# Kernel tuning notes

Measured on AMD Instinct MI355X. Metric: run time of the kernel, lower is better.

## Reference

```python
import jax, jax.numpy as jnp
import numpy as np

B = 4096
HASH_BITS = 128
TEACHER_DIM = 768
TEMPERATURE = 0.2
CONTRASTIVE_W = 1.0
DISTILL_W = 0.5
QUANT_W = 0.01


def _l2_normalize(x, eps=1e-12):
    # matches torch F.normalize(dim=-1)
    n = jnp.sqrt(jnp.sum(x * x, axis=-1, keepdims=True))
    return x / jnp.maximum(n, eps)


def setup_inputs() -> dict:
    key = jax.random.key(0)
    k1, k2, k3, k4 = jax.random.split(key, 4)
    logits = jax.random.normal(k1, (B, HASH_BITS), dtype=jnp.float32)
    # binary {-1,+1} codes as in the module contract
    hash_codes = jnp.sign(jax.random.normal(k2, (B, HASH_BITS), dtype=jnp.float32))
    hash_codes = jnp.where(hash_codes == 0, 1.0, hash_codes)
    teacher_embed = jax.random.normal(k3, (B, TEACHER_DIM), dtype=jnp.float32)
    # sparse random positives plus self-positives (guarantees each row nonempty)
    rand_pos = jax.random.uniform(k4, (B, B)) < 0.002
    eye = jnp.eye(B, dtype=bool)
    positive_mask = rand_pos | eye
    return {
        "logits": logits,
        "hash_codes": hash_codes,
        "teacher_embed": teacher_embed,
        "positive_mask": positive_mask,
    }


def reference(logits, hash_codes, teacher_embed, positive_mask):
    teacher = _l2_normalize(teacher_embed)

    # ---- contrastive (vectorized form of the per-row python loop) ----
    ln = _l2_normalize(logits)
    sim = (ln @ ln.T) / TEMPERATURE  # [B, B]
    eye = jnp.eye(sim.shape[0], dtype=bool)
    sim_masked = jnp.where(eye, -jnp.inf, sim)
    # per-row stable logsumexp over self-masked similarities
    log_denom = jax.nn.logsumexp(sim_masked, axis=1)  # [B]
    pm = positive_mask.astype(sim.dtype)
    cnt = pm.sum(axis=1)  # [B]
    pos_mean = (sim * pm).sum(axis=1) / jnp.maximum(cnt, 1.0)
    has_pos = cnt > 0
    per_row = jnp.where(has_pos, -pos_mean + log_denom, 0.0)
    num_pos = jnp.maximum(has_pos.sum(), 1)
    loss_cont = per_row.sum() / num_pos.astype(sim.dtype)

    # ---- distillation: hash similarity vs teacher similarity MSE ----
    hash_sim = (hash_codes @ hash_codes.T) / hash_codes.shape[-1]
    teacher_sim = teacher @ teacher.T
    loss_distill = jnp.mean((hash_sim - teacher_sim) ** 2)

    # ---- quantization: push |logits| toward 1 ----
    loss_quant = jnp.mean(jnp.abs(jnp.abs(logits) - 1.0))

    total = (
        CONTRASTIVE_W * loss_cont
        + DISTILL_W * loss_distill
        + QUANT_W * loss_quant
    )
    return total
```

## Files before the change

kernel.cpp:

```cpp
#include <hip/hip_runtime.h>


typedef __bf16 bf16x8 __attribute__((ext_vector_type(8)));
typedef float f32x4 __attribute__((ext_vector_type(4)));

__device__ __forceinline__ unsigned short f2bf(float f) {
  union { float f; unsigned int u; } v; v.f = f;
  unsigned int u = v.u;
  return (unsigned short)((u + 0x7FFFu + ((u >> 16) & 1u)) >> 16);
}

__global__ __launch_bounds__(256) void prep(const float* __restrict__ logits,
                                            const float* __restrict__ hash,
                                            const float* __restrict__ teacher,
                                            unsigned short* __restrict__ P,
                                            unsigned char* __restrict__ QT,
                                            float* __restrict__ qpart,
                                            float* __restrict__ rowexp,
                                            float* __restrict__ possum,
                                            float* __restrict__ cntw,
                                            float* __restrict__ dtot,
                                            float* __restrict__ Cbuf) {
  __shared__ float rnt[16];
  __shared__ unsigned char QL[16 * 897];
  const int t = threadIdx.x, wave = t >> 6, lane = t & 63;
  const int r0 = (int)blockIdx.x * 16;

  for (int i = t; i < 784; i += 256)
    *(f32x4*)&Cbuf[((size_t)blockIdx.x * 784 + i) * 4] = (f32x4){0.f, 0.f, 0.f, 0.f};

#pragma unroll
  for (int rr = 0; rr < 4; ++rr) {
    const int rl = wave * 4 + rr, r = r0 + rl;
    float ss = 0.f;
#pragma unroll
    for (int i = 0; i < 3; ++i) {
      const float4 v = *(const float4*)&teacher[(size_t)r * 768 + i * 256 + lane * 4];
      ss += v.x * v.x + v.y * v.y + v.z * v.z + v.w * v.w;
    }
    const float2 lv = *(const float2*)&logits[(size_t)r * 128 + lane * 2];
    float ssl = lv.x * lv.x + lv.y * lv.y;
    float qv = fabsf(fabsf(lv.x) - 1.f) + fabsf(fabsf(lv.y) - 1.f);
#pragma unroll
    for (int off = 1; off < 64; off <<= 1) {
      ss += __shfl_xor(ss, off, 64);
      ssl += __shfl_xor(ssl, off, 64);
      qv += __shfl_xor(qv, off, 64);
    }
    const float rnl = 1.f / fmaxf(sqrtf(ssl), 1e-12f);
    const unsigned int pk = (unsigned int)f2bf(lv.x * rnl) |
                            ((unsigned int)f2bf(lv.y * rnl) << 16);
    *(unsigned int*)&P[(size_t)r * 128 + lane * 2] = pk;
    if (lane == 0) {
      rnt[rl] = 11.313708498984761f / fmaxf(sqrtf(ss), 1e-12f);
      qpart[r] = qv;
    }
  }
  if (t < 16) { rowexp[r0 + t] = 0.f; possum[r0 + t] = 0.f; cntw[r0 + t] = 0.f; }
  if (blockIdx.x == 0 && t == 0) *dtot = 0.f;
  __syncthreads();

#pragma unroll
  for (int it = 0; it < 4; ++it) {
    const int task = it * 256 + t;
    if (task < 896) {
      const int r = task / 56, cb = task % 56;
      const int r_g = r0 + r;
      unsigned char* dst = &QL[r * 897 + cb * 16];
      if (cb < 8) {
        const float4 v0 = *(const float4*)&hash[(size_t)r_g * 128 + cb * 16];
        const float4 v1 = *(const float4*)&hash[(size_t)r_g * 128 + cb * 16 + 4];
        const float4 v2 = *(const float4*)&hash[(size_t)r_g * 128 + cb * 16 + 8];
        const float4 v3 = *(const float4*)&hash[(size_t)r_g * 128 + cb * 16 + 12];
        const float vv[16] = {v0.x, v0.y, v0.z, v0.w, v1.x, v1.y, v1.z, v1.w,
                              v2.x, v2.y, v2.z, v2.w, v3.x, v3.y, v3.z, v3.w};
#pragma unroll
        for (int k = 0; k < 16; ++k) dst[k] = vv[k] >= 0.f ? 0x38 : 0xB8;
      } else {
        const float sc = rnt[r];
        const int c0 = cb * 16 - 128;
        const float4 v0 = *(const float4*)&teacher[(size_t)r_g * 768 + c0];
        const float4 v1 = *(const float4*)&teacher[(size_t)r_g * 768 + c0 + 4];
        const float4 v2 = *(const float4*)&teacher[(size_t)r_g * 768 + c0 + 8];
        const float4 v3 = *(const float4*)&teacher[(size_t)r_g * 768 + c0 + 12];
        const float vv[16] = {v0.x, v0.y, v0.z, v0.w, v1.x, v1.y, v1.z, v1.w,
                              v2.x, v2.y, v2.z, v2.w, v3.x, v3.y, v3.z, v3.w};
#pragma unroll
        for (int k = 0; k < 16; ++k) {
          const int p8 = __builtin_amdgcn_cvt_pk_fp8_f32(vv[k] * sc, vv[k] * sc,
                                                         0, false);
          dst[k] = (unsigned char)(p8 & 0xFF);
        }
      }
    }
  }
  __syncthreads();

#pragma unroll
  for (int i = 0; i < 4; ++i) {
    const int c = t + 256 * i;
    if (c < 896) {
      unsigned char buf[16];
#pragma unroll
      for (int j = 0; j < 16; ++j) buf[j] = QL[j * 897 + c];
      *(uint4*)&QT[(size_t)c * 4096 + r0] = *(uint4*)buf;
    }
  }
}

#define STAGE_GEN(GA, GB, PITCH)                                               \
  {                                                                            \
    _Pragma("unroll") for (int it = 0; it < 4; ++it) {                         \
      const int task = it * 256 + t;                                           \
      const int row = task >> 3;                                               \
      const int c16 = (task & 7) ^ (row & 7);                                  \
      const unsigned char* gpA = (GA) + (size_t)row * (PITCH) + c16 * 16;      \
      __builtin_amdgcn_global_load_lds(                                        \
          (const __attribute__((address_space(1))) void*)gpA,                  \
          (__attribute__((address_space(3))) void*)&SB[it * 4096 + wave * 1024],\
          16, 0, 0);                                                           \
      if (offdiag) {                                                           \
        const unsigned char* gpB = (GB) + (size_t)row * (PITCH) + c16 * 16;    \
        __builtin_amdgcn_global_load_lds(                                      \
            (const __attribute__((address_space(1))) void*)gpB,                \
            (__attribute__((address_space(3)))                                 \
                 void*)&SB[16384 + it * 4096 + wave * 1024],                   \
            16, 0, 0);                                                         \
      }                                                                        \
    }                                                                          \
  }

#define MFMA_B()                                                               \
  {                                                                            \
    _Pragma("unroll") for (int ks = 0; ks < 2; ++ks) {                         \
      const int ph = ((ks * 4 + qd) ^ (l15 & 7)) * 16;                         \
      bf16x8 af[4], bfr[4];                                                    \
      _Pragma("unroll") for (int rt = 0; rt < 4; ++rt)                         \
          af[rt] = *(const bf16x8*)&SB[(wy * 64 + rt * 16 + l15) * 128 + ph];  \
      _Pragma("unroll") for (int ct = 0; ct < 4; ++ct)                         \
          bfr[ct] = *(const bf16x8*)&SB[boffB +                                \
                                        (wx * 64 + ct * 16 + l15) * 128 + ph]; \
      _Pragma("unroll") for (int rt = 0; rt < 4; ++rt)                         \
          _Pragma("unroll") for (int ct = 0; ct < 4; ++ct) acc[rt][ct] =       \
          __builtin_amdgcn_mfma_f32_16x16x32_bf16(af[rt], bfr[ct],             \
                                                  acc[rt][ct], 0, 0, 0);       \
    }                                                                          \
  }

#define MFMA_Q()                                                               \
  {                                                                            \
    _Pragma("unroll") for (int ks = 0; ks < 4; ++ks) {                         \
      const int g0 = ks * 4 + qd;                                              \
      const int ph = ((g0 >> 1) ^ (l15 & 7)) * 16 + (g0 & 1) * 8;              \
      long af[4], bfr[4];                                                      \
      _Pragma("unroll") for (int rt = 0; rt < 4; ++rt)                         \
          af[rt] = *(const long*)&SB[(wy * 64 + rt * 16 + l15) * 128 + ph];    \
      _Pragma("unroll") for (int ct = 0; ct < 4; ++ct)                         \
          bfr[ct] = *(const long*)&SB[boffB +                                  \
                                      (wx * 64 + ct * 16 + l15) * 128 + ph];   \
      _Pragma("unroll") for (int rt = 0; rt < 4; ++rt)                         \
          _Pragma("unroll") for (int ct = 0; ct < 4; ++ct) acc[rt][ct] =       \
          __builtin_amdgcn_mfma_f32_16x16x32_fp8_fp8(af[rt], bfr[ct],          \
                                                     acc[rt][ct], 0, 0, 0);    \
    }                                                                          \
  }

__global__ __launch_bounds__(256, 3) void mega(const unsigned short* __restrict__ P,
                                               const unsigned char* __restrict__ QT,
                                               const void* __restrict__ mask,
                                               float* __restrict__ rowexp,
                                               float* __restrict__ possum,
                                               float* __restrict__ cntw,
                                               float* __restrict__ Cbuf) {
  __shared__ __align__(16) unsigned char SB[32768];
  __shared__ __align__(16) unsigned char MD[16384];
  __shared__ float redrow[128][2];

  const int t = threadIdx.x;
  const int wave = t >> 6, lane = t & 63;
  const int qd = lane >> 4, l15 = lane & 15;
  const int wy = wave >> 1, wx = wave & 1;
  const int b = (int)blockIdx.x;

  f32x4 acc[4][4];
#pragma unroll
  for (int rt = 0; rt < 4; ++rt)
#pragma unroll
    for (int ct = 0; ct < 4; ++ct) acc[rt][ct] = {0.f, 0.f, 0.f, 0.f};

  if (b < 224) {
    const int tile = b % 28, ks = b / 28;
    int I = 0, rem = tile;
    while (rem >= 7 - I) { rem -= 7 - I; ++I; }
    const int J = I + rem;
    const bool offdiag = (I != J);
    const int boffB = offdiag ? 16384 : 0;
    const unsigned char* QA = QT + (size_t)I * 128 * 4096 + ks * 512;
    const unsigned char* QB = QT + (size_t)J * 128 * 4096 + ks * 512;
    for (int kc = 0; kc < 4; ++kc) {
      __syncthreads();
      STAGE_GEN(QA + kc * 128, QB + kc * 128, 4096);
      __syncthreads();
      MFMA_Q();
    }
    float* Ct = Cbuf + (size_t)I * 128 * 896 + J * 128;
#pragma unroll
    for (int rt = 0; rt < 4; ++rt) {
      const int row = wy * 64 + rt * 16 + qd * 4;
#pragma unroll
      for (int ct = 0; ct < 4; ++ct) {
        const int col = wx * 64 + ct * 16 + l15;
#pragma unroll
        for (int i = 0; i < 4; ++i)
          atomicAdd(&Ct[(size_t)(row + i) * 896 + col], acc[rt][ct][i]);
      }
    }
  } else {
    const int bb = b - 224;
    const int l = (bb & 7) * 128 + (bb >> 3);
    const int bi = l >> 5, bj = l & 31;
    const int ti = bi * 128, tj = bj * 128;
    const bool offdiag = (bi != bj);
    const int boffB = offdiag ? 16384 : 0;

    const bool is_byte = ((const unsigned char*)mask)[4097] != 0;
    if (is_byte) {
      const unsigned char* m8d = (const unsigned char*)mask + (size_t)ti * 4096 + tj;
#pragma unroll
      for (int it = 0; it < 4; ++it) {
        const int task = it * 256 + t;
        const int row = task >> 3, seg = task & 7;
        __builtin_amdgcn_global_load_lds(
            (const __attribute__((address_space(1))) void*)
                (m8d + (size_t)row * 4096 + seg * 16),
            (__attribute__((address_space(3))) void*)&MD[it * 4096 + wave * 1024],
            16, 0, 0);
      }
    }

    const unsigned char* Pa = (const unsigned char*)(P + (size_t)ti * 128);
    const unsigned char* Pb = (const unsigned char*)(P + (size_t)tj * 128);
    for (int kc = 0; kc < 2; ++kc) {
      __syncthreads();
      STAGE_GEN(Pa + kc * 128, Pb + kc * 128, 256);
      __syncthreads();
      MFMA_B();
    }

    __syncthreads();
    if (!is_byte) {
      const unsigned int* m32 = (const unsigned int*)mask;
#pragma unroll
      for (int it = 0; it < 16; ++it) {
        const int task = it * 256 + t;
        const int row = task >> 5, seg = task & 31;
        const uint4 v = *(const uint4*)&m32[(size_t)(ti + row) * 4096 + tj + seg * 4];
        uchar4 pk;
        pk.x = v.x ? 1 : 0; pk.y = v.y ? 1 : 0;
        pk.z = v.z ? 1 : 0; pk.w = v.w ? 1 : 0;
        *(uchar4*)&MD[row * 128 + seg * 4] = pk;
      }
      __syncthreads();
    }

#pragma unroll
    for (int rt = 0; rt < 4; ++rt) {
#pragma unroll
      for (int r = 0; r < 4; ++r) {
        const int mrow = wy * 64 + rt * 16 + qd * 4 + r;
        const int m = ti + mrow;
        float se = 0.f;
#pragma unroll
        for (int ct = 0; ct < 4; ++ct) {
          const int ncol = wx * 64 + ct * 16 + l15;
          const int n = tj + ncol;
          const float sim = acc[rt][ct][r] * 5.0f;
          const float e = __expf(sim);
          if (m != n) se += e;
          if (MD[mrow * 128 + ncol]) {
            atomicAdd(&possum[m], sim);
            atomicAdd(&cntw[m], 1.0f);
          }
        }
#pragma unroll
        for (int off = 1; off < 16; off <<= 1) se += __shfl_xor(se, off, 64);
        if (l15 == 0) redrow[mrow][wx] = se;
      }
    }
    __syncthreads();
    if (t < 128) atomicAdd(&rowexp[ti + t], redrow[t][0] + redrow[t][1]);
  }
}

__global__ __launch_bounds__(256) void gsq(const float* __restrict__ C,
                                           float* __restrict__ dtot) {
  const int t = threadIdx.x;
  const int wave = t >> 6, lane = t & 63;
  float s = 0.f;
  for (int q = (int)blockIdx.x * 256 + t; q < 200704; q += 256 * 256) {
    const f32x4 v = *(const f32x4*)&C[(size_t)q * 4];
    const int r = q / 224;
    const int c0 = (q - r * 224) * 4;
    const int Ir = r >> 7;
#pragma unroll
    for (int k = 0; k < 4; ++k) {
      const int Jc = (c0 + k) >> 7;
      const float w = (Ir == Jc) ? 1.f : 2.f;
      const float sg = ((Ir == 0) == (Jc == 0)) ? w : -w;
      s += sg * v[k] * v[k];
    }
  }
#pragma unroll
  for (int off = 1; off < 64; off <<= 1) s += __shfl_xor(s, off, 64);
  __shared__ float sw[4];
  if (lane == 0) sw[wave] = s;
  __syncthreads();
  if (t == 0) atomicAdd(dtot, sw[0] + sw[1] + sw[2] + sw[3]);
}

__global__ __launch_bounds__(1024) void finalize(const float* __restrict__ rowexp,
                                                 const float* __restrict__ possum,
                                                 const float* __restrict__ cnt,
                                                 const float* __restrict__ qpart,
                                                 const float* __restrict__ dtot,
                                                 float* __restrict__ out) {
  const int t = threadIdx.x;
  const int wave = t >> 6, lane = t & 63;
  float c = 0.f, q = 0.f;
  for (int m = t; m < 4096; m += 1024) {
    c += logf(rowexp[m]) - possum[m] / fmaxf(cnt[m], 1.0f);
    q += qpart[m];
  }
#pragma unroll
  for (int off = 1; off < 64; off <<= 1) {
    c += __shfl_xor(c, off, 64);
    q += __shfl_xor(q, off, 64);
  }
  __shared__ float sc[16], sq[16];
  if (lane == 0) { sc[wave] = c; sq[wave] = q; }
  __syncthreads();
  if (t == 0) {
    float C = 0.f, Q = 0.f;
    for (int i = 0; i < 16; ++i) { C += sc[i]; Q += sq[i]; }
    out[0] = C * (1.0f / 4096.0f) + 0.5f * (dtot[0] * 3.6379788e-12f) +
             0.01f * (Q * (1.0f / 524288.0f));
  }
}

extern "C" void kernel_launch(void* const* d_in, const int* in_sizes, int n_in,
                              void* d_out, int out_size, void* d_ws, size_t ws_size,
                              hipStream_t stream) {
  const float* logits = (const float*)d_in[0];
  const float* hash = (const float*)d_in[1];
  const float* teacher = (const float*)d_in[2];
  const void* mask = d_in[3];
  float* out = (float*)d_out;

  char* ws = (char*)d_ws;
  float* rowexp = (float*)(ws + 0);
  float* possum = (float*)(ws + 16384);
  float* cntw = (float*)(ws + 32768);
  float* qpart = (float*)(ws + 49152);
  float* dtot = (float*)(ws + 65536);
  unsigned short* P = (unsigned short*)(ws + 98304);
  unsigned char* QT = (unsigned char*)(ws + 98304 + 1048576);
  float* Cbuf = (float*)(ws + 98304 + 1048576 + 3670016);

  prep<<<256, 256, 0, stream>>>(logits, hash, teacher, P, QT, qpart, rowexp,
                                possum, cntw, dtot, Cbuf);
  mega<<<1248, 256, 0, stream>>>(P, QT, mask, rowexp, possum, cntw, Cbuf);
  gsq<<<256, 256, 0, stream>>>(Cbuf, dtot);
  finalize<<<1, 1024, 0, stream>>>(rowexp, possum, cntw, qpart, dtot, out);
}
```

Before: 153.4 us.

## Double-buffer LDS staging, replace split-K atomics with partial buffers

The LDS staging buffer grows to 64KB and is double-buffered, so global-to-LDS loads for the next K chunk overlap the MFMAs on the current one in both the fp8 Gram path and the bf16 similarity path. The mask staging buffer now reuses SB. The split-K Gram tiles are reduced from 8 to 4 K-slices, and each slice writes its accumulators with plain stores into a per-slice partial buffer instead of atomically adding into a zeroed C buffer. gsq then sums the partials before squaring, and the other float atomics switch to unsafeAtomicAdd. The cost is lower occupancy (launch bound 3 to 2 blocks per CU), fewer Gram blocks, and extra partial-buffer traffic in gsq.

```diff
diff --git a/kernel.cpp b/kernel.cpp
--- a/kernel.cpp
+++ b/kernel.cpp
@@ -8,6 +8,10 @@
   union { float f; unsigned int u; } v; v.f = f;
   unsigned int u = v.u;
   return (unsigned short)((u + 0x7FFFu + ((u >> 16) & 1u)) >> 16);
+}
+
+__device__ __forceinline__ void atomAddF(float* p, float v) {
+  unsafeAtomicAdd(p, v);
 }
 
 __global__ __launch_bounds__(256) void prep(const float* __restrict__ logits,
@@ -19,15 +23,11 @@
                                             float* __restrict__ rowexp,
                                             float* __restrict__ possum,
                                             float* __restrict__ cntw,
-                                            float* __restrict__ dtot,
-                                            float* __restrict__ Cbuf) {
+                                            float* __restrict__ dtot) {
   __shared__ float rnt[16];
   __shared__ unsigned char QL[16 * 897];
   const int t = threadIdx.x, wave = t >> 6, lane = t & 63;
   const int r0 = (int)blockIdx.x * 16;
-
-  for (int i = t; i < 784; i += 256)
-    *(f32x4*)&Cbuf[((size_t)blockIdx.x * 784 + i) * 4] = (f32x4){0.f, 0.f, 0.f, 0.f};
 
 #pragma unroll
   for (int rr = 0; rr < 4; ++rr) {
@@ -108,7 +108,7 @@
   }
 }
 
-#define STAGE_GEN(GA, GB, PITCH)                                               \
+#define STAGE_GEN(GA, GB, PITCH, BASE)                                         \
   {                                                                            \
     _Pragma("unroll") for (int it = 0; it < 4; ++it) {                         \
       const int task = it * 256 + t;                                           \
@@ -117,28 +117,30 @@
       const unsigned char* gpA = (GA) + (size_t)row * (PITCH) + c16 * 16;      \
       __builtin_amdgcn_global_load_lds(                                        \
           (const __attribute__((address_space(1))) void*)gpA,                  \
-          (__attribute__((address_space(3))) void*)&SB[it * 4096 + wave * 1024],\
+          (__attribute__((address_space(3))) void*)                            \
+              &SB[(BASE) + it * 4096 + wave * 1024],                           \
           16, 0, 0);                                                           \
       if (offdiag) {                                                           \
         const unsigned char* gpB = (GB) + (size_t)row * (PITCH) + c16 * 16;    \
         __builtin_amdgcn_global_load_lds(                                      \
             (const __attribute__((address_space(1))) void*)gpB,                \
-            (__attribute__((address_space(3)))                                 \
-                 void*)&SB[16384 + it * 4096 + wave * 1024],                   \
+            (__attribute__((address_space(3))) void*)                         \
+                &SB[(BASE) + 16384 + it * 4096 + wave * 1024],                 \
             16, 0, 0);                                                         \
       }                                                                        \
     }                                                                          \
   }
 
-#define MFMA_B()                                                               \
+#define MFMA_B(BASE)                                                           \
   {                                                                            \
     _Pragma("unroll") for (int ks = 0; ks < 2; ++ks) {                         \
       const int ph = ((ks * 4 + qd) ^ (l15 & 7)) * 16;                         \
       bf16x8 af[4], bfr[4];                                                    \
       _Pragma("unroll") for (int rt = 0; rt < 4; ++rt)                         \
-          af[rt] = *(const bf16x8*)&SB[(wy * 64 + rt * 16 + l15) * 128 + ph];  \
+          af[rt] = *(const bf16x8*)&SB[(BASE) +                                \
+                                       (wy * 64 + rt * 16 + l15) * 128 + ph];  \
       _Pragma("unroll") for (int ct = 0; ct < 4; ++ct)                         \
-          bfr[ct] = *(const bf16x8*)&SB[boffB +                                \
+          bfr[ct] = *(const bf16x8*)&SB[(BASE) + boffB +                       \
                                         (wx * 64 + ct * 16 + l15) * 128 + ph]; \
       _Pragma("unroll") for (int rt = 0; rt < 4; ++rt)                         \
           _Pragma("unroll") for (int ct = 0; ct < 4; ++ct) acc[rt][ct] =       \
@@ -147,16 +149,17 @@
     }                                                                          \
   }
 
-#define MFMA_Q()                                                               \
+#define MFMA_Q(BASE)                                                           \
   {                                                                            \
     _Pragma("unroll") for (int ks = 0; ks < 4; ++ks) {                         \
       const int g0 = ks * 4 + qd;                                              \
       const int ph = ((g0 >> 1) ^ (l15 & 7)) * 16 + (g0 & 1) * 8;              \
       long af[4], bfr[4];                                                      \
       _Pragma("unroll") for (int rt = 0; rt < 4; ++rt)                         \
-          af[rt] = *(const long*)&SB[(wy * 64 + rt * 16 + l15) * 128 + ph];    \
+          af[rt] = *(const long*)&SB[(BASE) +                                  \
+                                     (wy * 64 + rt * 16 + l15) * 128 + ph];    \
       _Pragma("unroll") for (int ct = 0; ct < 4; ++ct)                         \
-          bfr[ct] = *(const long*)&SB[boffB +                                  \
+          bfr[ct] = *(const long*)&SB[(BASE) + boffB +                         \
                                       (wx * 64 + ct * 16 + l15) * 128 + ph];   \
       _Pragma("unroll") for (int rt = 0; rt < 4; ++rt)                         \
           _Pragma("unroll") for (int ct = 0; ct < 4; ++ct) acc[rt][ct] =       \
@@ -165,15 +168,14 @@
     }                                                                          \
   }
 
-__global__ __launch_bounds__(256, 3) void mega(const unsigned short* __restrict__ P,
+__global__ __launch_bounds__(256, 2) void mega(const unsigned short* __restrict__ P,
                                                const unsigned char* __restrict__ QT,
                                                const void* __restrict__ mask,
                                                float* __restrict__ rowexp,
                                                float* __restrict__ possum,
                                                float* __restrict__ cntw,
-                                               float* __restrict__ Cbuf) {
-  __shared__ __align__(16) unsigned char SB[32768];
-  __shared__ __align__(16) unsigned char MD[16384];
+                                               float* __restrict__ Cpart) {
+  __shared__ __align__(16) unsigned char SB[65536];
   __shared__ float redrow[128][2];
 
   const int t = threadIdx.x;
@@ -188,42 +190,48 @@
 #pragma unroll
     for (int ct = 0; ct < 4; ++ct) acc[rt][ct] = {0.f, 0.f, 0.f, 0.f};
 
-  if (b < 224) {
-    const int tile = b % 28, ks = b / 28;
+  if (b < 112) {
+    const int tile = b >> 2, ksl = b & 3;
     int I = 0, rem = tile;
     while (rem >= 7 - I) { rem -= 7 - I; ++I; }
     const int J = I + rem;
     const bool offdiag = (I != J);
     const int boffB = offdiag ? 16384 : 0;
-    const unsigned char* QA = QT + (size_t)I * 128 * 4096 + ks * 512;
-    const unsigned char* QB = QT + (size_t)J * 128 * 4096 + ks * 512;
-    for (int kc = 0; kc < 4; ++kc) {
+    const unsigned char* QA = QT + (size_t)I * 128 * 4096 + ksl * 1024;
+    const unsigned char* QB = QT + (size_t)J * 128 * 4096 + ksl * 1024;
+
+    STAGE_GEN(QA, QB, 4096, 0);
+    __syncthreads();
+    for (int kc = 0; kc < 8; ++kc) {
+      const int cb = (kc & 1) * 32768;
+      if (kc < 7) STAGE_GEN(QA + (kc + 1) * 128, QB + (kc + 1) * 128, 4096,
+                            cb ^ 32768);
+      MFMA_Q(cb);
       __syncthreads();
-      STAGE_GEN(QA + kc * 128, QB + kc * 128, 4096);
-      __syncthreads();
-      MFMA_Q();
-    }
-    float* Ct = Cbuf + (size_t)I * 128 * 896 + J * 128;
-#pragma unroll
-    for (int rt = 0; rt < 4; ++rt) {
-      const int row = wy * 64 + rt * 16 + qd * 4;
-#pragma unroll
-      for (int ct = 0; ct < 4; ++ct) {
-        const int col = wx * 64 + ct * 16 + l15;
-#pragma unroll
-        for (int i = 0; i < 4; ++i)
-          atomicAdd(&Ct[(size_t)(row + i) * 896 + col], acc[rt][ct][i]);
-      }
-    }
+    }
+    float* Ct = Cpart + ((size_t)(tile * 4 + ksl)) * 16384 + t * 64;
+#pragma unroll
+    for (int rt = 0; rt < 4; ++rt)
+#pragma unroll
+      for (int ct = 0; ct < 4; ++ct)
+        *(f32x4*)&Ct[(rt * 4 + ct) * 4] = acc[rt][ct];
   } else {
-    const int bb = b - 224;
+    const int bb = b - 112;
     const int l = (bb & 7) * 128 + (bb >> 3);
     const int bi = l >> 5, bj = l & 31;
     const int ti = bi * 128, tj = bj * 128;
     const bool offdiag = (bi != bj);
     const int boffB = offdiag ? 16384 : 0;
-
     const bool is_byte = ((const unsigned char*)mask)[4097] != 0;
+
+    const unsigned char* Pa = (const unsigned char*)(P + (size_t)ti * 128);
+    const unsigned char* Pb = (const unsigned char*)(P + (size_t)tj * 128);
+
+    STAGE_GEN(Pa, Pb, 256, 0);
+    __syncthreads();
+    STAGE_GEN(Pa + 128, Pb + 128, 256, 32768);
+    MFMA_B(0);
+    __syncthreads();
     if (is_byte) {
       const unsigned char* m8d = (const unsigned char*)mask + (size_t)ti * 4096 + tj;
 #pragma unroll
@@ -233,20 +241,11 @@
         __builtin_amdgcn_global_load_lds(
             (const __attribute__((address_space(1))) void*)
                 (m8d + (size_t)row * 4096 + seg * 16),
-            (__attribute__((address_space(3))) void*)&MD[it * 4096 + wave * 1024],
+            (__attribute__((address_space(3))) void*)&SB[it * 4096 + wave * 1024],
             16, 0, 0);
       }
     }
-
-    const unsigned char* Pa = (const unsigned char*)(P + (size_t)ti * 128);
-    const unsigned char* Pb = (const unsigned char*)(P + (size_t)tj * 128);
-    for (int kc = 0; kc < 2; ++kc) {
-      __syncthreads();
-      STAGE_GEN(Pa + kc * 128, Pb + kc * 128, 256);
-      __syncthreads();
-      MFMA_B();
-    }
-
+    MFMA_B(32768);
     __syncthreads();
     if (!is_byte) {
       const unsigned int* m32 = (const unsigned int*)mask;
@@ -258,7 +257,7 @@
         uchar4 pk;
         pk.x = v.x ? 1 : 0; pk.y = v.y ? 1 : 0;
         pk.z = v.z ? 1 : 0; pk.w = v.w ? 1 : 0;
-        *(uchar4*)&MD[row * 128 + seg * 4] = pk;
+        *(uchar4*)&SB[row * 128 + seg * 4] = pk;
       }
       __syncthreads();
     }
@@ -277,9 +276,9 @@
           const float sim = acc[rt][ct][r] * 5.0f;
           const float e = __expf(sim);
           if (m != n) se += e;
-          if (MD[mrow * 128 + ncol]) {
-            atomicAdd(&possum[m], sim);
-            atomicAdd(&cntw[m], 1.0f);
+          if (SB[mrow * 128 + ncol]) {
+            atomAddF(&possum[m], sim);
+            atomAddF(&cntw[m], 1.0f);
           }
         }
 #pragma unroll
@@ -288,34 +287,33 @@
       }
     }
     __syncthreads();
-    if (t < 128) atomicAdd(&rowexp[ti + t], redrow[t][0] + redrow[t][1]);
-  }
-}
-
-__global__ __launch_bounds__(256) void gsq(const float* __restrict__ C,
+    if (t < 128) atomAddF(&rowexp[ti + t], redrow[t][0] + redrow[t][1]);
+  }
+}
+
+__global__ __launch_bounds__(256) void gsq(const float* __restrict__ Cpart,
                                            float* __restrict__ dtot) {
   const int t = threadIdx.x;
   const int wave = t >> 6, lane = t & 63;
   float s = 0.f;
-  for (int q = (int)blockIdx.x * 256 + t; q < 200704; q += 256 * 256) {
-    const f32x4 v = *(const f32x4*)&C[(size_t)q * 4];
-    const int r = q / 224;
-    const int c0 = (q - r * 224) * 4;
-    const int Ir = r >> 7;
-#pragma unroll
-    for (int k = 0; k < 4; ++k) {
-      const int Jc = (c0 + k) >> 7;
-      const float w = (Ir == Jc) ? 1.f : 2.f;
-      const float sg = ((Ir == 0) == (Jc == 0)) ? w : -w;
-      s += sg * v[k] * v[k];
-    }
+  for (int e = (int)blockIdx.x * 256 + t; e < 458752; e += 448 * 256) {
+    const int tile = e >> 14, idx = e & 16383;
+    int I = 0, rem = tile;
+    while (rem >= 7 - I) { rem -= 7 - I; ++I; }
+    const int J = I + rem;
+    float v = 0.f;
+#pragma unroll
+    for (int k = 0; k < 4; ++k)
+      v += Cpart[((size_t)(tile * 4 + k)) * 16384 + idx];
+    const float w = (I == J ? 1.f : 2.f) * (((I == 0) == (J == 0)) ? 1.f : -1.f);
+    s += w * v * v;
   }
 #pragma unroll
   for (int off = 1; off < 64; off <<= 1) s += __shfl_xor(s, off, 64);
   __shared__ float sw[4];
   if (lane == 0) sw[wave] = s;
   __syncthreads();
-  if (t == 0) atomicAdd(dtot, sw[0] + sw[1] + sw[2] + sw[3]);
+  if (t == 0) atomAddF(dtot, sw[0] + sw[1] + sw[2] + sw[3]);
 }
 
 __global__ __launch_bounds__(1024) void finalize(const float* __restrict__ rowexp,
@@ -364,11 +362,11 @@
   float* dtot = (float*)(ws + 65536);
   unsigned short* P = (unsigned short*)(ws + 98304);
   unsigned char* QT = (unsigned char*)(ws + 98304 + 1048576);
-  float* Cbuf = (float*)(ws + 98304 + 1048576 + 3670016);
+  float* Cpart = (float*)(ws + 98304 + 1048576 + 3670016);
 
   prep<<<256, 256, 0, stream>>>(logits, hash, teacher, P, QT, qpart, rowexp,
-                                possum, cntw, dtot, Cbuf);
-  mega<<<1248, 256, 0, stream>>>(P, QT, mask, rowexp, possum, cntw, Cbuf);
-  gsq<<<256, 256, 0, stream>>>(Cbuf, dtot);
+                                possum, cntw, dtot);
+  mega<<<1136, 256, 0, stream>>>(P, QT, mask, rowexp, possum, cntw, Cpart);
+  gsq<<<448, 256, 0, stream>>>(Cpart, dtot);
   finalize<<<1, 1024, 0, stream>>>(rowexp, possum, cntw, qpart, dtot, out);
 }
```

Measured after the change: 156.5 us. 1.02x slower.
